# Kernel optimization log

Measured on AMD Instinct MI355X. Metric: run time of the kernel, lower is better.

Reference implementation:

```python
import jax, jax.numpy as jnp
import numpy as np

N_NODES = 50000
N_EDGES = 800000


def graph_conv(h, W, b, src, dst, n_nodes):
    # DGL GraphConv with norm='both':
    #   out = D_in^{-1/2} * A^T * (D_out^{-1/2} * h) @ W + b
    ones = jnp.ones((src.shape[0],), dtype=h.dtype)
    deg_out = jax.ops.segment_sum(ones, src, num_segments=n_nodes)
    deg_in = jax.ops.segment_sum(ones, dst, num_segments=n_nodes)
    norm_src = jnp.clip(deg_out, 1.0) ** -0.5  # [N]
    norm_dst = jnp.clip(deg_in, 1.0) ** -0.5   # [N]
    msg = (h * norm_src[:, None])[src]          # [E, F] gather
    agg = jax.ops.segment_sum(msg, dst, num_segments=n_nodes)  # [N, F] scatter
    return (agg * norm_dst[:, None]) @ W + b


def setup_inputs() -> dict:
    key = jax.random.key(0)
    ks = jax.random.split(key, 5)
    h = jax.random.normal(ks[0], (N_NODES, 64), dtype=jnp.float32)
    src = jax.random.randint(ks[1], (N_EDGES,), 0, N_NODES, dtype=jnp.int32)
    dst = jax.random.randint(ks[2], (N_EDGES,), 0, N_NODES, dtype=jnp.int32)
    W1 = jax.random.normal(ks[3], (64, 128), dtype=jnp.float32) * (1.0 / np.sqrt(64))
    b1 = jnp.zeros((128,), dtype=jnp.float32)
    W2 = jax.random.normal(ks[4], (128, 64), dtype=jnp.float32) * (1.0 / np.sqrt(128))
    b2 = jnp.zeros((64,), dtype=jnp.float32)
    return {"h": h, "src": src, "dst": dst, "W1": W1, "b1": b1, "W2": W2, "b2": b2}


def reference(h, src, dst, W1, b1, W2, b2):
    n = h.shape[0]
    h1 = jax.nn.relu(graph_conv(h, W1, b1, src, dst, n))
    out = graph_conv(h1, W2, b2, src, dst, n)
    return out
```

## Files before the change

### kernel.cpp

```cpp
#include <hip/hip_runtime.h>


#define NBMAX 512
#define CAPLOG 12
#define CAP (1 << CAPLOG)

typedef __attribute__((ext_vector_type(8))) short bf16x8;
typedef __attribute__((ext_vector_type(4))) float f32x4;

__device__ inline unsigned short f2bf(float f) {
    unsigned int u = __float_as_uint(f);
    unsigned int r = (u + 0x7FFFu + ((u >> 16) & 1u)) >> 16;
    return (unsigned short)r;
}
__device__ inline float bf2f_lo(unsigned int u) { return __uint_as_float(u << 16); }
__device__ inline float bf2f_hi(unsigned int u) { return __uint_as_float(u & 0xFFFF0000u); }

__global__ __launch_bounds__(256) void place_direct(const int* __restrict__ src,
        const int* __restrict__ dst, int* __restrict__ cnt_s, int* __restrict__ cnt_d,
        unsigned char* __restrict__ ss, unsigned int* __restrict__ sd,
        int n_edges, int nb,
        const float* __restrict__ W1, const float* __restrict__ W2,
        unsigned short* __restrict__ w1t_g, unsigned short* __restrict__ w2t_g) {
    if (blockIdx.x == gridDim.x - 1) {
        for (int i = threadIdx.x; i < 8192; i += 256) {
            int k = i >> 7, nn = i & 127;
            w1t_g[nn * 72 + k] = f2bf(W1[i]);
        }
        for (int i = threadIdx.x; i < 8192; i += 256) {
            int k = i >> 6, nn = i & 63;
            w2t_g[nn * 136 + k] = f2bf(W2[i]);
        }
        return;
    }
    __shared__ int hs[NBMAX], hd[NBMAX], bs[NBMAX], bd[NBMAX];
    for (int i = threadIdx.x; i < nb; i += 256) { hs[i] = 0; hd[i] = 0; }
    __syncthreads();
    const int nact = gridDim.x - 1;
    int chunk = (n_edges + nact - 1) / nact;
    int e0 = blockIdx.x * chunk;
    int e1 = e0 + chunk; if (e1 > n_edges) e1 = n_edges;
    for (int e = e0 + (int)threadIdx.x; e < e1; e += 256) {
        atomicAdd(&hs[src[e] >> 7], 1);
        atomicAdd(&hd[dst[e] >> 7], 1);
    }
    __syncthreads();
    for (int i = threadIdx.x; i < nb; i += 256) {
        int v = hs[i]; bs[i] = v ? atomicAdd(&cnt_s[i], v) : 0; hs[i] = 0;
        v = hd[i];     bd[i] = v ? atomicAdd(&cnt_d[i], v) : 0; hd[i] = 0;
    }
    __syncthreads();
    for (int e = e0 + (int)threadIdx.x; e < e1; e += 256) {
        int s = src[e], d = dst[e];
        int sb = s >> 7, db = d >> 7;
        int ps = bs[sb] + atomicAdd(&hs[sb], 1);
        ss[((size_t)sb << CAPLOG) + ps] = (unsigned char)(s & 127);
        int pd = bd[db] + atomicAdd(&hd[db], 1);
        sd[((size_t)db << CAPLOG) + pd] = ((unsigned int)(d & 127) << 25) | (unsigned int)s;
    }
}

__global__ __launch_bounds__(256) void prep(const float* __restrict__ h,
        const unsigned char* __restrict__ ss, const int* __restrict__ cnt_s,
        const unsigned int* __restrict__ sd, const int* __restrict__ cnt_d,
        float* __restrict__ norm_src, unsigned short* __restrict__ xb,
        int2* __restrict__ node_rng, unsigned short* __restrict__ srt,
        float* __restrict__ norm_dst, int n) {
    __shared__ int cnt[128], cur[128];
    __shared__ float nrm[128];
    __shared__ int w0tot;
    const int b = blockIdx.x;
    const int tid = threadIdx.x;

    if (tid < 128) cnt[tid] = 0;
    __syncthreads();
    {
        int used = cnt_s[b];
        const unsigned char* p = ss + ((size_t)b << CAPLOG);
        for (int i = tid; i < used; i += 256) atomicAdd(&cnt[p[i]], 1);
    }
    __syncthreads();
    if (tid < 128) {
        int c = cnt[tid]; if (c < 1) c = 1;
        float s = 1.0f / sqrtf((float)c);
        nrm[tid] = s;
        int node = (b << 7) + tid;
        if (node < n) norm_src[node] = s;
    }
    __syncthreads();
    {
        int base = b << 7;
        for (int t = tid; t < 128 * 16; t += 256) {
            int r = t >> 4, c4 = (t & 15) << 2;
            int node = base + r;
            if (node < n) {
                float s = nrm[r];
                float4 v = *(const float4*)(h + (size_t)node * 64 + c4);
                ushort4 o;
                o.x = f2bf(v.x * s); o.y = f2bf(v.y * s);
                o.z = f2bf(v.z * s); o.w = f2bf(v.w * s);
                *(ushort4*)(xb + (size_t)node * 64 + c4) = o;
            }
        }
    }
    __syncthreads();

    if (tid < 128) cnt[tid] = 0;
    __syncthreads();
    int used = cnt_d[b];
    const unsigned int* p = sd + ((size_t)b << CAPLOG);
    for (int i = tid; i < used; i += 256) atomicAdd(&cnt[p[i] >> 25], 1);
    __syncthreads();
    int lane = tid & 63, wid = tid >> 6;
    int v = (tid < 128) ? cnt[tid] : 0;
    int incl = v;
    #pragma unroll
    for (int d = 1; d < 64; d <<= 1) {
        int t = __shfl_up(incl, d, 64);
        if (lane >= d) incl += t;
    }
    if (tid == 63) w0tot = incl;
    __syncthreads();
    if (tid < 128) {
        int excl = incl - v + (wid == 1 ? w0tot : 0);
        cur[tid] = excl;
        int node = (b << 7) + tid;
        if (node < n) {
            int base = b << CAPLOG;
            node_rng[node] = make_int2(base + excl, base + excl + v);
            int c = v; if (c < 1) c = 1;
            norm_dst[node] = 1.0f / sqrtf((float)c);
        }
    }
    __syncthreads();
    for (int i = tid; i < used; i += 256) {
        unsigned int e = p[i];
        int l = (int)(e >> 25);
        int pos = atomicAdd(&cur[l], 1);
        srt[((size_t)b << CAPLOG) + pos] = (unsigned short)(e & 0xFFFFu);
    }
}

__global__ __launch_bounds__(256) void gather24(const unsigned short* __restrict__ xb,
        const unsigned short* __restrict__ srt, const int2* __restrict__ node_rng,
        const float* __restrict__ nrm, const float* __restrict__ bias,
        void* __restrict__ outp, int write_bf, int n_nodes) {
    int node = blockIdx.x * 4 + (threadIdx.x >> 6);
    if (node >= n_nodes) return;
    int lane = threadIdx.x & 63;
    int g  = lane >> 3;
    int c8 = (lane & 7) * 8;
    int2 rng = node_rng[node];
    int a0 = rng.x, a1 = rng.y;
    float acc[8];
    #pragma unroll
    for (int j = 0; j < 8; ++j) acc[j] = 0.f;
    for (int base = a0; base < a1; base += 24) {
        #pragma unroll
        for (int u = 0; u < 3; ++u) {
            int ei = base + u * 8 + g;
            int idx = ei < a1 ? ei : a1 - 1;
            float msk = ei < a1 ? 1.0f : 0.0f;
            int s = srt[idx];
            const uint4 v = *(const uint4*)(xb + (size_t)s * 64 + c8);
            acc[0] = fmaf(bf2f_lo(v.x), msk, acc[0]);
            acc[1] = fmaf(bf2f_hi(v.x), msk, acc[1]);
            acc[2] = fmaf(bf2f_lo(v.y), msk, acc[2]);
            acc[3] = fmaf(bf2f_hi(v.y), msk, acc[3]);
            acc[4] = fmaf(bf2f_lo(v.z), msk, acc[4]);
            acc[5] = fmaf(bf2f_hi(v.z), msk, acc[5]);
            acc[6] = fmaf(bf2f_lo(v.w), msk, acc[6]);
            acc[7] = fmaf(bf2f_hi(v.w), msk, acc[7]);
        }
    }
    #pragma unroll
    for (int off = 8; off < 64; off <<= 1) {
        #pragma unroll
        for (int j = 0; j < 8; ++j) acc[j] += __shfl_xor(acc[j], off, 64);
    }
    if (g == 0) {
        float s = nrm[node];
        float r[8];
        #pragma unroll
        for (int j = 0; j < 8; ++j) r[j] = acc[j] * s;
        if (write_bf) {
            unsigned short rb[8];
            #pragma unroll
            for (int j = 0; j < 8; ++j) rb[j] = f2bf(r[j]);
            unsigned short* o = (unsigned short*)outp + (size_t)node * 64 + c8;
            *(ushort4*)(o)     = make_ushort4(rb[0], rb[1], rb[2], rb[3]);
            *(ushort4*)(o + 4) = make_ushort4(rb[4], rb[5], rb[6], rb[7]);
        } else {
            if (bias) {
                #pragma unroll
                for (int j = 0; j < 8; ++j) r[j] += bias[c8 + j];
            }
            float* o = (float*)outp + (size_t)node * 64 + c8;
            *(float4*)(o)     = make_float4(r[0], r[1], r[2], r[3]);
            *(float4*)(o + 4) = make_float4(r[4], r[5], r[6], r[7]);
        }
    }
}

__global__ __launch_bounds__(256) void gemm12(const unsigned short* __restrict__ Ab,
        const unsigned short* __restrict__ w1t_g, const float* __restrict__ b1,
        const float* __restrict__ norm, const unsigned short* __restrict__ w2t_g,
        unsigned short* __restrict__ y2b, int n) {
    __shared__ __align__(16) unsigned short W1t[128 * 72];
    __shared__ __align__(16) unsigned short W2t[64 * 136];
    __shared__ __align__(16) unsigned short Hs[64 * 136];
    __shared__ float b1s[128];
    const int tid = threadIdx.x;

    {
        const uint4* s1 = (const uint4*)w1t_g;
        uint4* d1 = (uint4*)W1t;
        for (int i = tid; i < 1152; i += 256) d1[i] = s1[i];
        const uint4* s2 = (const uint4*)w2t_g;
        uint4* d2 = (uint4*)W2t;
        for (int i = tid; i < 1088; i += 256) d2[i] = s2[i];
    }
    if (tid < 128) b1s[tid] = b1[tid];
    __syncthreads();

    const int w  = tid >> 6;
    const int l  = tid & 63;
    const int ln = l & 15;
    const int q  = l >> 4;
    const int m0 = blockIdx.x * 64 + w * 16;

    int arow = m0 + ln; if (arow > n - 1) arow = n - 1;
    const unsigned short* arp = Ab + (size_t)arow * 64 + q * 8;
    bf16x8 a0 = *(const bf16x8*)(arp);
    bf16x8 a1 = *(const bf16x8*)(arp + 32);

    float ns[4];
    #pragma unroll
    for (int r = 0; r < 4; ++r) {
        int node = m0 + q * 4 + r;
        ns[r] = norm[node < n ? node : n - 1];
    }

    #pragma unroll
    for (int c = 0; c < 8; ++c) {
        const unsigned short* bp = W1t + (c * 16 + ln) * 72 + q * 8;
        bf16x8 b0 = *(const bf16x8*)(bp);
        bf16x8 bk = *(const bf16x8*)(bp + 32);
        f32x4 acc = {0.f, 0.f, 0.f, 0.f};
        acc = __builtin_amdgcn_mfma_f32_16x16x32_bf16(a0, b0, acc, 0, 0, 0);
        acc = __builtin_amdgcn_mfma_f32_16x16x32_bf16(a1, bk, acc, 0, 0, 0);
        int col = c * 16 + ln;
        float bb = b1s[col];
        #pragma unroll
        for (int r = 0; r < 4; ++r) {
            float v = acc[r] + bb;
            v = v > 0.f ? v : 0.f;
            Hs[(w * 16 + q * 4 + r) * 136 + col] = f2bf(v * ns[r]);
        }
    }
    __syncthreads();

    const unsigned short* hp = Hs + (size_t)(w * 16 + ln) * 136 + q * 8;
    bf16x8 h0 = *(const bf16x8*)(hp);
    bf16x8 h1 = *(const bf16x8*)(hp + 32);
    bf16x8 h2 = *(const bf16x8*)(hp + 64);
    bf16x8 h3 = *(const bf16x8*)(hp + 96);
    #pragma unroll
    for (int c = 0; c < 4; ++c) {
        const unsigned short* bp = W2t + (c * 16 + ln) * 136 + q * 8;
        f32x4 acc = {0.f, 0.f, 0.f, 0.f};
        acc = __builtin_amdgcn_mfma_f32_16x16x32_bf16(h0, *(const bf16x8*)(bp),      acc, 0, 0, 0);
        acc = __builtin_amdgcn_mfma_f32_16x16x32_bf16(h1, *(const bf16x8*)(bp + 32), acc, 0, 0, 0);
        acc = __builtin_amdgcn_mfma_f32_16x16x32_bf16(h2, *(const bf16x8*)(bp + 64), acc, 0, 0, 0);
        acc = __builtin_amdgcn_mfma_f32_16x16x32_bf16(h3, *(const bf16x8*)(bp + 96), acc, 0, 0, 0);
        #pragma unroll
        for (int r = 0; r < 4; ++r) {
            int node = m0 + q * 4 + r;
            if (node < n)
                y2b[(size_t)node * 64 + c * 16 + ln] = f2bf(acc[r]);
        }
    }
}

extern "C" void kernel_launch(void* const* d_in, const int* in_sizes, int n_in,
                              void* d_out, int out_size, void* d_ws, size_t ws_size,
                              hipStream_t stream) {
    const float* h   = (const float*)d_in[0];
    const int*   src = (const int*)d_in[1];
    const int*   dst = (const int*)d_in[2];
    const float* W1  = (const float*)d_in[3];
    const float* b1  = (const float*)d_in[4];
    const float* W2  = (const float*)d_in[5];
    const float* b2  = (const float*)d_in[6];
    float* out = (float*)d_out;

    const int n = in_sizes[0] / 64;
    const int E = in_sizes[1];
    const int nb = (n + 127) >> 7;

    char* p = (char*)d_ws;
    auto alloc = [&](size_t bytes) {
        void* r = (void*)p;
        p += (bytes + 255) & ~(size_t)255;
        return r;
    };
    float* norm_src      = (float*)alloc((size_t)n * 4);
    float* norm_dst      = (float*)alloc((size_t)n * 4);
    int2* node_rng       = (int2*)alloc((size_t)n * 8);
    int* cnt2            = (int*)alloc((size_t)2 * nb * 4);
    int* cnt_s = cnt2;
    int* cnt_d = cnt2 + nb;
    unsigned int* sd     = (unsigned int*)alloc((size_t)nb * CAP * 4);
    unsigned short* xb   = (unsigned short*)alloc((size_t)n * 64 * 2);
    unsigned short* agg1b= (unsigned short*)alloc((size_t)n * 64 * 2);
    unsigned short* y2b  = (unsigned short*)alloc((size_t)n * 64 * 2);
    unsigned short* srt  = (unsigned short*)alloc((size_t)nb * CAP * 2);
    unsigned char* ssb   = (unsigned char*)alloc((size_t)nb * CAP);
    unsigned short* w1t_g= (unsigned short*)alloc((size_t)128 * 72 * 2);
    unsigned short* w2t_g= (unsigned short*)alloc((size_t)64 * 136 * 2);

    hipMemsetAsync(cnt2, 0, 2 * (size_t)nb * sizeof(int), stream);

    place_direct<<<257, 256, 0, stream>>>(src, dst, cnt_s, cnt_d, ssb, sd,
                                          E, nb, W1, W2, w1t_g, w2t_g);
    prep<<<nb, 256, 0, stream>>>(h, ssb, cnt_s, sd, cnt_d, norm_src, xb,
                                 node_rng, srt, norm_dst, n);

    int gb = (n + 3) / 4;
    gather24<<<gb, 256, 0, stream>>>(xb, srt, node_rng, norm_dst, nullptr,
                                     (void*)agg1b, 1, n);

    int tb = (n + 63) / 64;
    gemm12<<<tb, 256, 0, stream>>>(agg1b, w1t_g, b1, norm_src, w2t_g, y2b, n);

    gather24<<<gb, 256, 0, stream>>>(y2b, srt, node_rng, norm_dst, b2,
                                     (void*)out, 0, n);
}
```

Measured before the change: 175.5 us.

## Replace global atomic bucket placement with histogram, scan, scatter passes

Splits edge bucketing into three kernels: per-block histograms written to global memory, a per-bucket prefix scan over blocks, and a scatter that uses the precomputed offsets. This removes the global atomicAdd reservation on bucket counters and the memset, and makes placement deterministic. In exchange it adds two extra kernel launches and reads src/dst twice across separate kernels, plus extra workspace traffic for hist/offs.

```diff
diff --git a/kernel.cpp b/kernel.cpp
--- a/kernel.cpp
+++ b/kernel.cpp
@@ -4,6 +4,7 @@
 #define NBMAX 512
 #define CAPLOG 12
 #define CAP (1 << CAPLOG)
+#define NB_BIN 256
 
 typedef __attribute__((ext_vector_type(8))) short bf16x8;
 typedef __attribute__((ext_vector_type(4))) float f32x4;
@@ -16,10 +17,8 @@
 __device__ inline float bf2f_lo(unsigned int u) { return __uint_as_float(u << 16); }
 __device__ inline float bf2f_hi(unsigned int u) { return __uint_as_float(u & 0xFFFF0000u); }
 
-__global__ __launch_bounds__(256) void place_direct(const int* __restrict__ src,
-        const int* __restrict__ dst, int* __restrict__ cnt_s, int* __restrict__ cnt_d,
-        unsigned char* __restrict__ ss, unsigned int* __restrict__ sd,
-        int n_edges, int nb,
+__global__ __launch_bounds__(256) void hist_edges(const int* __restrict__ src,
+        const int* __restrict__ dst, int* __restrict__ hist, int n_edges, int nb,
         const float* __restrict__ W1, const float* __restrict__ W2,
         unsigned short* __restrict__ w1t_g, unsigned short* __restrict__ w2t_g) {
     if (blockIdx.x == gridDim.x - 1) {
@@ -33,11 +32,10 @@
         }
         return;
     }
-    __shared__ int hs[NBMAX], hd[NBMAX], bs[NBMAX], bd[NBMAX];
+    __shared__ int hs[NBMAX], hd[NBMAX];
     for (int i = threadIdx.x; i < nb; i += 256) { hs[i] = 0; hd[i] = 0; }
     __syncthreads();
-    const int nact = gridDim.x - 1;
-    int chunk = (n_edges + nact - 1) / nact;
+    int chunk = (n_edges + NB_BIN - 1) / NB_BIN;
     int e0 = blockIdx.x * chunk;
     int e1 = e0 + chunk; if (e1 > n_edges) e1 = n_edges;
     for (int e = e0 + (int)threadIdx.x; e < e1; e += 256) {
@@ -45,17 +43,60 @@
         atomicAdd(&hd[dst[e] >> 7], 1);
     }
     __syncthreads();
+    int* rs = hist + (size_t)blockIdx.x * NBMAX;
+    int* rd = hist + (size_t)(NB_BIN + blockIdx.x) * NBMAX;
+    for (int i = threadIdx.x; i < nb; i += 256) { rs[i] = hs[i]; rd[i] = hd[i]; }
+}
+
+__global__ __launch_bounds__(256) void scan_hist(const int* __restrict__ hist,
+        int* __restrict__ offs, int* __restrict__ cnt_s, int* __restrict__ cnt_d,
+        int nb) {
+    __shared__ int wtot[4];
+    int j = blockIdx.x;
+    int side = j >= nb ? 1 : 0;
+    int bucket = j - side * nb;
+    const int tid = threadIdx.x;
+    size_t idx = (size_t)(side * NB_BIN + tid) * NBMAX + bucket;
+    int v = hist[idx];
+    int lane = tid & 63, wid = tid >> 6;
+    int incl = v;
+    #pragma unroll
+    for (int d = 1; d < 64; d <<= 1) {
+        int t = __shfl_up(incl, d, 64);
+        if (lane >= d) incl += t;
+    }
+    if (lane == 63) wtot[wid] = incl;
+    __syncthreads();
+    int pre = 0;
+    #pragma unroll
+    for (int k = 0; k < 3; ++k) if (k < wid) pre += wtot[k];
+    int excl = pre + incl - v;
+    offs[idx] = excl;
+    if (tid == 255) {
+        int tot = excl + v;
+        if (side) cnt_d[bucket] = tot; else cnt_s[bucket] = tot;
+    }
+}
+
+__global__ __launch_bounds__(256) void scatter_binned(const int* __restrict__ src,
+        const int* __restrict__ dst, const int* __restrict__ offs,
+        unsigned char* __restrict__ ss, unsigned int* __restrict__ sd,
+        int n_edges, int nb) {
+    __shared__ int cs[NBMAX], cd[NBMAX];
     for (int i = threadIdx.x; i < nb; i += 256) {
-        int v = hs[i]; bs[i] = v ? atomicAdd(&cnt_s[i], v) : 0; hs[i] = 0;
-        v = hd[i];     bd[i] = v ? atomicAdd(&cnt_d[i], v) : 0; hd[i] = 0;
-    }
-    __syncthreads();
+        cs[i] = offs[(size_t)blockIdx.x * NBMAX + i];
+        cd[i] = offs[(size_t)(NB_BIN + blockIdx.x) * NBMAX + i];
+    }
+    __syncthreads();
+    int chunk = (n_edges + NB_BIN - 1) / NB_BIN;
+    int e0 = blockIdx.x * chunk;
+    int e1 = e0 + chunk; if (e1 > n_edges) e1 = n_edges;
     for (int e = e0 + (int)threadIdx.x; e < e1; e += 256) {
         int s = src[e], d = dst[e];
         int sb = s >> 7, db = d >> 7;
-        int ps = bs[sb] + atomicAdd(&hs[sb], 1);
+        int ps = atomicAdd(&cs[sb], 1);
         ss[((size_t)sb << CAPLOG) + ps] = (unsigned char)(s & 127);
-        int pd = bd[db] + atomicAdd(&hd[db], 1);
+        int pd = atomicAdd(&cd[db], 1);
         sd[((size_t)db << CAPLOG) + pd] = ((unsigned int)(d & 127) << 25) | (unsigned int)s;
     }
 }
@@ -307,9 +348,10 @@
     float* norm_src      = (float*)alloc((size_t)n * 4);
     float* norm_dst      = (float*)alloc((size_t)n * 4);
     int2* node_rng       = (int2*)alloc((size_t)n * 8);
-    int* cnt2            = (int*)alloc((size_t)2 * nb * 4);
-    int* cnt_s = cnt2;
-    int* cnt_d = cnt2 + nb;
+    int* cnt_s           = (int*)alloc((size_t)nb * 4);
+    int* cnt_d           = (int*)alloc((size_t)nb * 4);
+    int* hist            = (int*)alloc((size_t)2 * NB_BIN * NBMAX * 4);
+    int* offs            = (int*)alloc((size_t)2 * NB_BIN * NBMAX * 4);
     unsigned int* sd     = (unsigned int*)alloc((size_t)nb * CAP * 4);
     unsigned short* xb   = (unsigned short*)alloc((size_t)n * 64 * 2);
     unsigned short* agg1b= (unsigned short*)alloc((size_t)n * 64 * 2);
@@ -319,10 +361,10 @@
     unsigned short* w1t_g= (unsigned short*)alloc((size_t)128 * 72 * 2);
     unsigned short* w2t_g= (unsigned short*)alloc((size_t)64 * 136 * 2);
 
-    hipMemsetAsync(cnt2, 0, 2 * (size_t)nb * sizeof(int), stream);
-
-    place_direct<<<257, 256, 0, stream>>>(src, dst, cnt_s, cnt_d, ssb, sd,
-                                          E, nb, W1, W2, w1t_g, w2t_g);
+    hist_edges<<<NB_BIN + 1, 256, 0, stream>>>(src, dst, hist, E, nb,
+                                               W1, W2, w1t_g, w2t_g);
+    scan_hist<<<2 * nb, 256, 0, stream>>>(hist, offs, cnt_s, cnt_d, nb);
+    scatter_binned<<<NB_BIN, 256, 0, stream>>>(src, dst, offs, ssb, sd, E, nb);
     prep<<<nb, 256, 0, stream>>>(h, ssb, cnt_s, sd, cnt_d, norm_src, xb,
                                  node_rng, srt, norm_dst, n);
 
```

Measured after the change: 173.3 us. About the same (-1.2%).

## Replace global-atomic edge binning with cooperative kernel and deterministic prefix offsets

Applied to the files above, without the earlier changes.

Edge bucketing now runs as a single cooperative kernel with 1024 blocks. Each block writes its per-bucket histogram to global memory, then after a grid sync one block per bucket scans across blocks to get exclusive offsets and totals. After a second grid sync each block scatters its edges using those offsets. This removes the global atomics on bucket counters and the memset, and spreads the edge work over more blocks, at the cost of two grid-wide barriers and extra global traffic for the histogram and offset arrays.

```diff
diff --git a/kernel.cpp b/kernel.cpp
--- a/kernel.cpp
+++ b/kernel.cpp
@@ -1,9 +1,11 @@
 #include <hip/hip_runtime.h>
+#include <hip/hip_cooperative_groups.h>
 
 
 #define NBMAX 512
 #define CAPLOG 12
 #define CAP (1 << CAPLOG)
+#define NBLK2 1024
 
 typedef __attribute__((ext_vector_type(8))) short bf16x8;
 typedef __attribute__((ext_vector_type(4))) float f32x4;
@@ -16,46 +18,94 @@
 __device__ inline float bf2f_lo(unsigned int u) { return __uint_as_float(u << 16); }
 __device__ inline float bf2f_hi(unsigned int u) { return __uint_as_float(u & 0xFFFF0000u); }
 
-__global__ __launch_bounds__(256) void place_direct(const int* __restrict__ src,
-        const int* __restrict__ dst, int* __restrict__ cnt_s, int* __restrict__ cnt_d,
+__global__ __launch_bounds__(256, 4) void bin_coop(
+        const int* __restrict__ src, const int* __restrict__ dst,
+        int* __restrict__ hist, int* __restrict__ offs,
+        int* __restrict__ cnt_s, int* __restrict__ cnt_d,
         unsigned char* __restrict__ ss, unsigned int* __restrict__ sd,
         int n_edges, int nb,
         const float* __restrict__ W1, const float* __restrict__ W2,
         unsigned short* __restrict__ w1t_g, unsigned short* __restrict__ w2t_g) {
-    if (blockIdx.x == gridDim.x - 1) {
-        for (int i = threadIdx.x; i < 8192; i += 256) {
-            int k = i >> 7, nn = i & 127;
-            w1t_g[nn * 72 + k] = f2bf(W1[i]);
-        }
-        for (int i = threadIdx.x; i < 8192; i += 256) {
-            int k = i >> 6, nn = i & 63;
-            w2t_g[nn * 136 + k] = f2bf(W2[i]);
-        }
-        return;
-    }
-    __shared__ int hs[NBMAX], hd[NBMAX], bs[NBMAX], bd[NBMAX];
-    for (int i = threadIdx.x; i < nb; i += 256) { hs[i] = 0; hd[i] = 0; }
-    __syncthreads();
-    const int nact = gridDim.x - 1;
-    int chunk = (n_edges + nact - 1) / nact;
-    int e0 = blockIdx.x * chunk;
+    cooperative_groups::grid_group grid = cooperative_groups::this_grid();
+    __shared__ int hs[NBMAX], hd[NBMAX];
+    __shared__ int wtot[4];
+    const int bid = blockIdx.x;
+    const int tid = threadIdx.x;
+    int chunk = (n_edges + NBLK2 - 1) / NBLK2;
+    int e0 = bid * chunk;
     int e1 = e0 + chunk; if (e1 > n_edges) e1 = n_edges;
-    for (int e = e0 + (int)threadIdx.x; e < e1; e += 256) {
+
+    for (int i = tid; i < nb; i += 256) { hs[i] = 0; hd[i] = 0; }
+    __syncthreads();
+    for (int e = e0 + tid; e < e1; e += 256) {
         atomicAdd(&hs[src[e] >> 7], 1);
         atomicAdd(&hd[dst[e] >> 7], 1);
     }
     __syncthreads();
-    for (int i = threadIdx.x; i < nb; i += 256) {
-        int v = hs[i]; bs[i] = v ? atomicAdd(&cnt_s[i], v) : 0; hs[i] = 0;
-        v = hd[i];     bd[i] = v ? atomicAdd(&cnt_d[i], v) : 0; hd[i] = 0;
-    }
-    __syncthreads();
-    for (int e = e0 + (int)threadIdx.x; e < e1; e += 256) {
+    for (int i = tid; i < nb; i += 256) {
+        hist[(size_t)bid * NBMAX + i] = hs[i];
+        hist[(size_t)(NBLK2 + bid) * NBMAX + i] = hd[i];
+    }
+    grid.sync();
+
+    if (bid < 2 * nb) {
+        int side = bid >= nb ? 1 : 0;
+        int bucket = bid - side * nb;
+        size_t b0 = (size_t)(side * NBLK2 + tid * 4) * NBMAX + bucket;
+        int v0 = hist[b0];
+        int v1 = hist[b0 + NBMAX];
+        int v2 = hist[b0 + 2 * NBMAX];
+        int v3 = hist[b0 + 3 * NBMAX];
+        int s = v0 + v1 + v2 + v3;
+        int lane = tid & 63, wid = tid >> 6;
+        int incl = s;
+        #pragma unroll
+        for (int d = 1; d < 64; d <<= 1) {
+            int t = __shfl_up(incl, d, 64);
+            if (lane >= d) incl += t;
+        }
+        if (lane == 63) wtot[wid] = incl;
+        __syncthreads();
+        int pre = 0;
+        #pragma unroll
+        for (int k = 0; k < 3; ++k) if (k < wid) pre += wtot[k];
+        int eb = pre + incl - s;
+        offs[b0]             = eb;
+        offs[b0 + NBMAX]     = eb + v0;
+        offs[b0 + 2 * NBMAX] = eb + v0 + v1;
+        offs[b0 + 3 * NBMAX] = eb + v0 + v1 + v2;
+        if (tid == 255) {
+            int tot = eb + s;
+            if (side) cnt_d[bucket] = tot; else cnt_s[bucket] = tot;
+        }
+    }
+    {
+        int wb0 = (2 * nb + 2 <= NBLK2) ? 2 * nb : 0;
+        if (bid == wb0) {
+            for (int i = tid; i < 8192; i += 256) {
+                int k = i >> 7, nn = i & 127;
+                w1t_g[nn * 72 + k] = f2bf(W1[i]);
+            }
+        } else if (bid == wb0 + 1) {
+            for (int i = tid; i < 8192; i += 256) {
+                int k = i >> 6, nn = i & 63;
+                w2t_g[nn * 136 + k] = f2bf(W2[i]);
+            }
+        }
+    }
+    grid.sync();
+
+    for (int i = tid; i < nb; i += 256) {
+        hs[i] = offs[(size_t)bid * NBMAX + i];
+        hd[i] = offs[(size_t)(NBLK2 + bid) * NBMAX + i];
+    }
+    __syncthreads();
+    for (int e = e0 + tid; e < e1; e += 256) {
         int s = src[e], d = dst[e];
         int sb = s >> 7, db = d >> 7;
-        int ps = bs[sb] + atomicAdd(&hs[sb], 1);
+        int ps = atomicAdd(&hs[sb], 1);
         ss[((size_t)sb << CAPLOG) + ps] = (unsigned char)(s & 127);
-        int pd = bd[db] + atomicAdd(&hd[db], 1);
+        int pd = atomicAdd(&hd[db], 1);
         sd[((size_t)db << CAPLOG) + pd] = ((unsigned int)(d & 127) << 25) | (unsigned int)s;
     }
 }
@@ -307,9 +357,10 @@
     float* norm_src      = (float*)alloc((size_t)n * 4);
     float* norm_dst      = (float*)alloc((size_t)n * 4);
     int2* node_rng       = (int2*)alloc((size_t)n * 8);
-    int* cnt2            = (int*)alloc((size_t)2 * nb * 4);
-    int* cnt_s = cnt2;
-    int* cnt_d = cnt2 + nb;
+    int* cnt_s           = (int*)alloc((size_t)nb * 4);
+    int* cnt_d           = (int*)alloc((size_t)nb * 4);
+    int* hist            = (int*)alloc((size_t)2 * NBLK2 * NBMAX * 4);
+    int* offs            = (int*)alloc((size_t)2 * NBLK2 * NBMAX * 4);
     unsigned int* sd     = (unsigned int*)alloc((size_t)nb * CAP * 4);
     unsigned short* xb   = (unsigned short*)alloc((size_t)n * 64 * 2);
     unsigned short* agg1b= (unsigned short*)alloc((size_t)n * 64 * 2);
@@ -319,10 +370,18 @@
     unsigned short* w1t_g= (unsigned short*)alloc((size_t)128 * 72 * 2);
     unsigned short* w2t_g= (unsigned short*)alloc((size_t)64 * 136 * 2);
 
-    hipMemsetAsync(cnt2, 0, 2 * (size_t)nb * sizeof(int), stream);
-
-    place_direct<<<257, 256, 0, stream>>>(src, dst, cnt_s, cnt_d, ssb, sd,
-                                          E, nb, W1, W2, w1t_g, w2t_g);
+    {
+        int E_ = E, nb_ = nb;
+        void* args[] = {
+            (void*)&src, (void*)&dst, (void*)&hist, (void*)&offs,
+            (void*)&cnt_s, (void*)&cnt_d, (void*)&ssb, (void*)&sd,
+            (void*)&E_, (void*)&nb_, (void*)&W1, (void*)&W2,
+            (void*)&w1t_g, (void*)&w2t_g
+        };
+        hipLaunchCooperativeKernel((const void*)bin_coop, dim3(NBLK2), dim3(256),
+                                   args, 0, stream);
+    }
+
     prep<<<nb, 256, 0, stream>>>(h, ssb, cnt_s, sd, cnt_d, norm_src, xb,
                                  node_rng, srt, norm_dst, n);
 
```

Measured after the change: 383.4 us. 2.18x slower.

## Fuse first-layer gather with both GEMMs into one kernel

Applied to the files above, without the earlier changes.

Merges the first-layer neighbour aggregation with the dense W1/ReLU/W2 stage, so each 64-node block gathers its rows into shared memory and feeds them straight into MFMA. This drops the agg1b intermediate round trip through global memory and one kernel launch, and weights are now read from global/L2 instead of being staged in LDS. The cost is lower gather parallelism: each wave now processes 16 nodes one after another instead of one node per wave across many blocks, which may hurt latency hiding. The final gather also loses its bf16-output path and always adds bias.

```diff
diff --git a/kernel.cpp b/kernel.cpp
--- a/kernel.cpp
+++ b/kernel.cpp
@@ -141,10 +141,129 @@
     }
 }
 
+__global__ __launch_bounds__(256) void gather_gemm(const unsigned short* __restrict__ xb,
+        const unsigned short* __restrict__ srt, const int2* __restrict__ node_rng,
+        const float* __restrict__ nrm_dst, const float* __restrict__ nrm_src,
+        const unsigned short* __restrict__ w1t_g, const float* __restrict__ b1,
+        const unsigned short* __restrict__ w2t_g, unsigned short* __restrict__ y2b,
+        int n) {
+    __shared__ __align__(16) unsigned short Hin[64 * 72];
+    __shared__ __align__(16) unsigned short Hs[64 * 136];
+    __shared__ float b1s[128];
+    const int tid = threadIdx.x;
+    const int w  = tid >> 6;
+    const int l  = tid & 63;
+    const int g  = l >> 3;
+    const int c8 = (l & 7) * 8;
+    const int mw = blockIdx.x * 64 + w * 16;
+
+    if (tid < 128) b1s[tid] = b1[tid];
+
+    for (int i = 0; i < 16; ++i) {
+        int node = mw + i;
+        int a0 = 0, a1 = 0;
+        float s = 0.f;
+        if (node < n) {
+            int2 rng = node_rng[node];
+            a0 = rng.x; a1 = rng.y;
+            s = nrm_dst[node];
+        }
+        float acc[8];
+        #pragma unroll
+        for (int j = 0; j < 8; ++j) acc[j] = 0.f;
+        for (int base = a0; base < a1; base += 24) {
+            #pragma unroll
+            for (int u = 0; u < 3; ++u) {
+                int ei = base + u * 8 + g;
+                int idx = ei < a1 ? ei : a1 - 1;
+                float msk = ei < a1 ? 1.0f : 0.0f;
+                int sidx = srt[idx];
+                const uint4 v = *(const uint4*)(xb + (size_t)sidx * 64 + c8);
+                acc[0] = fmaf(bf2f_lo(v.x), msk, acc[0]);
+                acc[1] = fmaf(bf2f_hi(v.x), msk, acc[1]);
+                acc[2] = fmaf(bf2f_lo(v.y), msk, acc[2]);
+                acc[3] = fmaf(bf2f_hi(v.y), msk, acc[3]);
+                acc[4] = fmaf(bf2f_lo(v.z), msk, acc[4]);
+                acc[5] = fmaf(bf2f_hi(v.z), msk, acc[5]);
+                acc[6] = fmaf(bf2f_lo(v.w), msk, acc[6]);
+                acc[7] = fmaf(bf2f_hi(v.w), msk, acc[7]);
+            }
+        }
+        #pragma unroll
+        for (int off = 8; off < 64; off <<= 1) {
+            #pragma unroll
+            for (int j = 0; j < 8; ++j) acc[j] += __shfl_xor(acc[j], off, 64);
+        }
+        if (g == 0) {
+            unsigned short rb[8];
+            #pragma unroll
+            for (int j = 0; j < 8; ++j) rb[j] = f2bf(acc[j] * s);
+            unsigned short* o = Hin + (size_t)(w * 16 + i) * 72 + c8;
+            *(ushort4*)(o)     = make_ushort4(rb[0], rb[1], rb[2], rb[3]);
+            *(ushort4*)(o + 4) = make_ushort4(rb[4], rb[5], rb[6], rb[7]);
+        }
+    }
+    __syncthreads();
+
+    const int ln = l & 15;
+    const int q  = l >> 4;
+
+    const unsigned short* arp = Hin + (size_t)(w * 16 + ln) * 72 + q * 8;
+    bf16x8 a0 = *(const bf16x8*)(arp);
+    bf16x8 a1 = *(const bf16x8*)(arp + 32);
+
+    float ns[4];
+    #pragma unroll
+    for (int r = 0; r < 4; ++r) {
+        int node = mw + q * 4 + r;
+        ns[r] = nrm_src[node < n ? node : n - 1];
+    }
+
+    #pragma unroll
+    for (int c = 0; c < 8; ++c) {
+        const unsigned short* bp = w1t_g + (c * 16 + ln) * 72 + q * 8;
+        bf16x8 b0 = *(const bf16x8*)(bp);
+        bf16x8 bk = *(const bf16x8*)(bp + 32);
+        f32x4 acc = {0.f, 0.f, 0.f, 0.f};
+        acc = __builtin_amdgcn_mfma_f32_16x16x32_bf16(a0, b0, acc, 0, 0, 0);
+        acc = __builtin_amdgcn_mfma_f32_16x16x32_bf16(a1, bk, acc, 0, 0, 0);
+        int col = c * 16 + ln;
+        float bb = b1s[col];
+        #pragma unroll
+        for (int r = 0; r < 4; ++r) {
+            float v = acc[r] + bb;
+            v = v > 0.f ? v : 0.f;
+            Hs[(w * 16 + q * 4 + r) * 136 + col] = f2bf(v * ns[r]);
+        }
+    }
+    __syncthreads();
+
+    const unsigned short* hp = Hs + (size_t)(w * 16 + ln) * 136 + q * 8;
+    bf16x8 h0 = *(const bf16x8*)(hp);
+    bf16x8 h1 = *(const bf16x8*)(hp + 32);
+    bf16x8 h2 = *(const bf16x8*)(hp + 64);
+    bf16x8 h3 = *(const bf16x8*)(hp + 96);
+    #pragma unroll
+    for (int c = 0; c < 4; ++c) {
+        const unsigned short* bp = w2t_g + (c * 16 + ln) * 136 + q * 8;
+        f32x4 acc = {0.f, 0.f, 0.f, 0.f};
+        acc = __builtin_amdgcn_mfma_f32_16x16x32_bf16(h0, *(const bf16x8*)(bp),      acc, 0, 0, 0);
+        acc = __builtin_amdgcn_mfma_f32_16x16x32_bf16(h1, *(const bf16x8*)(bp + 32), acc, 0, 0, 0);
+        acc = __builtin_amdgcn_mfma_f32_16x16x32_bf16(h2, *(const bf16x8*)(bp + 64), acc, 0, 0, 0);
+        acc = __builtin_amdgcn_mfma_f32_16x16x32_bf16(h3, *(const bf16x8*)(bp + 96), acc, 0, 0, 0);
+        #pragma unroll
+        for (int r = 0; r < 4; ++r) {
+            int node = mw + q * 4 + r;
+            if (node < n)
+                y2b[(size_t)node * 64 + c * 16 + ln] = f2bf(acc[r]);
+        }
+    }
+}
+
 __global__ __launch_bounds__(256) void gather24(const unsigned short* __restrict__ xb,
         const unsigned short* __restrict__ srt, const int2* __restrict__ node_rng,
         const float* __restrict__ nrm, const float* __restrict__ bias,
-        void* __restrict__ outp, int write_bf, int n_nodes) {
+        float* __restrict__ outp, int n_nodes) {
     int node = blockIdx.x * 4 + (threadIdx.x >> 6);
     if (node >= n_nodes) return;
     int lane = threadIdx.x & 63;
@@ -182,103 +301,10 @@
         float s = nrm[node];
         float r[8];
         #pragma unroll
-        for (int j = 0; j < 8; ++j) r[j] = acc[j] * s;
-        if (write_bf) {
-            unsigned short rb[8];
-            #pragma unroll
-            for (int j = 0; j < 8; ++j) rb[j] = f2bf(r[j]);
-            unsigned short* o = (unsigned short*)outp + (size_t)node * 64 + c8;
-            *(ushort4*)(o)     = make_ushort4(rb[0], rb[1], rb[2], rb[3]);
-            *(ushort4*)(o + 4) = make_ushort4(rb[4], rb[5], rb[6], rb[7]);
-        } else {
-            if (bias) {
-                #pragma unroll
-                for (int j = 0; j < 8; ++j) r[j] += bias[c8 + j];
-            }
-            float* o = (float*)outp + (size_t)node * 64 + c8;
-            *(float4*)(o)     = make_float4(r[0], r[1], r[2], r[3]);
-            *(float4*)(o + 4) = make_float4(r[4], r[5], r[6], r[7]);
-        }
-    }
-}
-
-__global__ __launch_bounds__(256) void gemm12(const unsigned short* __restrict__ Ab,
-        const unsigned short* __restrict__ w1t_g, const float* __restrict__ b1,
-        const float* __restrict__ norm, const unsigned short* __restrict__ w2t_g,
-        unsigned short* __restrict__ y2b, int n) {
-    __shared__ __align__(16) unsigned short W1t[128 * 72];
-    __shared__ __align__(16) unsigned short W2t[64 * 136];
-    __shared__ __align__(16) unsigned short Hs[64 * 136];
-    __shared__ float b1s[128];
-    const int tid = threadIdx.x;
-
-    {
-        const uint4* s1 = (const uint4*)w1t_g;
-        uint4* d1 = (uint4*)W1t;
-        for (int i = tid; i < 1152; i += 256) d1[i] = s1[i];
-        const uint4* s2 = (const uint4*)w2t_g;
-        uint4* d2 = (uint4*)W2t;
-        for (int i = tid; i < 1088; i += 256) d2[i] = s2[i];
-    }
-    if (tid < 128) b1s[tid] = b1[tid];
-    __syncthreads();
-
-    const int w  = tid >> 6;
-    const int l  = tid & 63;
-    const int ln = l & 15;
-    const int q  = l >> 4;
-    const int m0 = blockIdx.x * 64 + w * 16;
-
-    int arow = m0 + ln; if (arow > n - 1) arow = n - 1;
-    const unsigned short* arp = Ab + (size_t)arow * 64 + q * 8;
-    bf16x8 a0 = *(const bf16x8*)(arp);
-    bf16x8 a1 = *(const bf16x8*)(arp + 32);
-
-    float ns[4];
-    #pragma unroll
-    for (int r = 0; r < 4; ++r) {
-        int node = m0 + q * 4 + r;
-        ns[r] = norm[node < n ? node : n - 1];
-    }
-
-    #pragma unroll
-    for (int c = 0; c < 8; ++c) {
-        const unsigned short* bp = W1t + (c * 16 + ln) * 72 + q * 8;
-        bf16x8 b0 = *(const bf16x8*)(bp);
-        bf16x8 bk = *(const bf16x8*)(bp + 32);
-        f32x4 acc = {0.f, 0.f, 0.f, 0.f};
-        acc = __builtin_amdgcn_mfma_f32_16x16x32_bf16(a0, b0, acc, 0, 0, 0);
-        acc = __builtin_amdgcn_mfma_f32_16x16x32_bf16(a1, bk, acc, 0, 0, 0);
-        int col = c * 16 + ln;
-        float bb = b1s[col];
-        #pragma unroll
-        for (int r = 0; r < 4; ++r) {
-            float v = acc[r] + bb;
-            v = v > 0.f ? v : 0.f;
-            Hs[(w * 16 + q * 4 + r) * 136 + col] = f2bf(v * ns[r]);
-        }
-    }
-    __syncthreads();
-
-    const unsigned short* hp = Hs + (size_t)(w * 16 + ln) * 136 + q * 8;
-    bf16x8 h0 = *(const bf16x8*)(hp);
-    bf16x8 h1 = *(const bf16x8*)(hp + 32);
-    bf16x8 h2 = *(const bf16x8*)(hp + 64);
-    bf16x8 h3 = *(const bf16x8*)(hp + 96);
-    #pragma unroll
-    for (int c = 0; c < 4; ++c) {
-        const unsigned short* bp = W2t + (c * 16 + ln) * 136 + q * 8;
-        f32x4 acc = {0.f, 0.f, 0.f, 0.f};
-        acc = __builtin_amdgcn_mfma_f32_16x16x32_bf16(h0, *(const bf16x8*)(bp),      acc, 0, 0, 0);
-        acc = __builtin_amdgcn_mfma_f32_16x16x32_bf16(h1, *(const bf16x8*)(bp + 32), acc, 0, 0, 0);
-        acc = __builtin_amdgcn_mfma_f32_16x16x32_bf16(h2, *(const bf16x8*)(bp + 64), acc, 0, 0, 0);
-        acc = __builtin_amdgcn_mfma_f32_16x16x32_bf16(h3, *(const bf16x8*)(bp + 96), acc, 0, 0, 0);
-        #pragma unroll
-        for (int r = 0; r < 4; ++r) {
-            int node = m0 + q * 4 + r;
-            if (node < n)
-                y2b[(size_t)node * 64 + c * 16 + ln] = f2bf(acc[r]);
-        }
+        for (int j = 0; j < 8; ++j) r[j] = fmaf(acc[j], s, bias[c8 + j]);
+        float* o = outp + (size_t)node * 64 + c8;
+        *(float4*)(o)     = make_float4(r[0], r[1], r[2], r[3]);
+        *(float4*)(o + 4) = make_float4(r[4], r[5], r[6], r[7]);
     }
 }
 
@@ -312,7 +338,6 @@
     int* cnt_d = cnt2 + nb;
     unsigned int* sd     = (unsigned int*)alloc((size_t)nb * CAP * 4);
     unsigned short* xb   = (unsigned short*)alloc((size_t)n * 64 * 2);
-    unsigned short* agg1b= (unsigned short*)alloc((size_t)n * 64 * 2);
     unsigned short* y2b  = (unsigned short*)alloc((size_t)n * 64 * 2);
     unsigned short* srt  = (unsigned short*)alloc((size_t)nb * CAP * 2);
     unsigned char* ssb   = (unsigned char*)alloc((size_t)nb * CAP);
@@ -326,13 +351,10 @@
     prep<<<nb, 256, 0, stream>>>(h, ssb, cnt_s, sd, cnt_d, norm_src, xb,
                                  node_rng, srt, norm_dst, n);
 
+    int tb = (n + 63) / 64;
+    gather_gemm<<<tb, 256, 0, stream>>>(xb, srt, node_rng, norm_dst, norm_src,
+                                        w1t_g, b1, w2t_g, y2b, n);
+
     int gb = (n + 3) / 4;
-    gather24<<<gb, 256, 0, stream>>>(xb, srt, node_rng, norm_dst, nullptr,
-                                     (void*)agg1b, 1, n);
-
-    int tb = (n + 63) / 64;
-    gemm12<<<tb, 256, 0, stream>>>(agg1b, w1t_g, b1, norm_src, w2t_g, y2b, n);
-
-    gather24<<<gb, 256, 0, stream>>>(y2b, srt, node_rng, norm_dst, b2,
-                                     (void*)out, 0, n);
-}
+    gather24<<<gb, 256, 0, stream>>>(y2b, srt, node_rng, norm_dst, b2, out, n);
+}
```

Result: no change. 176.2 us (+0.4%).
